# Optimization experiments

Measured on AMD Instinct MI355X. Metric: run time of the kernel, lower is better.

## Reference

```python
import jax, jax.numpy as jnp
import numpy as np

B, NP, NG = 4, 8192, 8192

def setup_inputs() -> dict:
    key = jax.random.key(0)
    k1, k2, k3 = jax.random.split(key, 3)
    pr_pts = jax.random.normal(k1, (B, NP, 3), dtype=jnp.float32)
    gt_pts = jax.random.normal(k2, (B, NG, 3), dtype=jnp.float32)
    gt_valid = jax.random.randint(k3, (B, NG), 0, 2) > 0
    return {"pr_pts": pr_pts, "gt_pts": gt_pts, "gt_valid": gt_valid}

def _sq_dists(a, b):
    # a: [B,N,3], b: [B,M,3] -> squared pairwise distances [B,N,M]
    a2 = jnp.sum(a * a, -1)  # [B,N]
    b2 = jnp.sum(b * b, -1)  # [B,M]
    ab = jnp.einsum('bnd,bmd->bnm', a, b)
    return a2[:, :, None] + b2[:, None, :] - 2.0 * ab

def reference(pr_pts, gt_pts, gt_valid):
    # Bidirectional Chamfer distance with gt validity mask.
    d2 = _sq_dists(pr_pts, gt_pts)  # [B,Np,Ng]
    # accuracy: for each predicted point, min squared dist to a VALID gt point
    d2_masked = jnp.where(gt_valid[:, None, :], d2, jnp.inf)
    acc_b = jnp.mean(jnp.min(d2_masked, axis=-1), axis=-1)  # [B]
    # completeness: for each valid gt point, min squared dist to any pred point
    min_over_pr = jnp.min(d2, axis=1)  # [B,Ng]
    valid_f = gt_valid.astype(min_over_pr.dtype)
    com_b = jnp.sum(min_over_pr * valid_f, axis=-1) / jnp.maximum(jnp.sum(valid_f, axis=-1), 1.0)
    loss_acc = jnp.mean(acc_b)
    loss_com = jnp.mean(com_b)
    loss_cd = loss_acc + loss_com
    # Sum((loss_acc,None),(loss_com,None),(loss_cd,None)) with scalar losses -> acc+com+cd
    return loss_acc + loss_com + loss_cd
```

## Files before the change

kernel.cpp:

```cpp
#include <hip/hip_runtime.h>

#define BB 4
#define NN 8192

typedef _Float16 f16;
typedef _Float16 f16x8 __attribute__((ext_vector_type(8)));
typedef float f32x16 __attribute__((ext_vector_type(16)));

#define SZ_PACK (BB * NN * 16)
#define OFF_PART_BYTES (4 * SZ_PACK * 2)
#define OFF_RES_BYTES (OFF_PART_BYTES + 16 * NN * 4)

__global__ __launch_bounds__(256) void k_init(
    const float* __restrict__ pr, const float* __restrict__ gt,
    const int* __restrict__ valid,
    f16* __restrict__ APR, f16* __restrict__ BGT,
    f16* __restrict__ AGT, f16* __restrict__ BPR,
    float* __restrict__ res) {
  int i = blockIdx.x * 256 + threadIdx.x;
  if (blockIdx.x == 0 && threadIdx.x < 16) res[threadIdx.x] = 0.0f;
  if (i >= BB * NN) return;
  float px = pr[3 * i], py = pr[3 * i + 1], pz = pr[3 * i + 2];
  float gx = gt[3 * i], gy = gt[3 * i + 1], gz = gt[3 * i + 2];
  int vld = valid[i] != 0;

  f16 phx = (f16)px, phy = (f16)py, phz = (f16)pz;
  f16 plx = (f16)(px - (float)phx), ply = (f16)(py - (float)phy), plz = (f16)(pz - (float)phz);
  float p2 = px * px + py * py + pz * pz;
  f16 p2h = (f16)p2, p2l = (f16)(p2 - (float)p2h);

  f16 ghx = (f16)gx, ghy = (f16)gy, ghz = (f16)gz;
  f16 glx = (f16)(gx - (float)ghx), gly = (f16)(gy - (float)ghy), glz = (f16)(gz - (float)ghz);
  float g2 = gx * gx + gy * gy + gz * gz;
  f16 g2h = (f16)g2, g2l = (f16)(g2 - (float)g2h);
  f16 g2hm = vld ? g2h : (f16)32768.0f;
  f16 g2lm = vld ? g2l : (f16)0.0f;

  const f16 one = (f16)1.0f, zero = (f16)0.0f;
  union Rec { f16 h[16]; uint4 u[2]; };

  Rec ra;
  ra.h[0] = (f16)(-2.f * (float)phx); ra.h[1] = (f16)(-2.f * (float)phy); ra.h[2] = (f16)(-2.f * (float)phz);
  ra.h[3] = ra.h[0]; ra.h[4] = ra.h[1]; ra.h[5] = ra.h[2];
  ra.h[6] = (f16)(-2.f * (float)plx); ra.h[7] = (f16)(-2.f * (float)ply); ra.h[8] = (f16)(-2.f * (float)plz);
  ra.h[9] = p2h; ra.h[10] = p2l; ra.h[11] = one; ra.h[12] = one;
  ra.h[13] = zero; ra.h[14] = zero; ra.h[15] = zero;
  ((uint4*)APR)[2 * i] = ra.u[0]; ((uint4*)APR)[2 * i + 1] = ra.u[1];

  Rec rb;
  rb.h[0] = phx; rb.h[1] = phy; rb.h[2] = phz;
  rb.h[3] = plx; rb.h[4] = ply; rb.h[5] = plz;
  rb.h[6] = phx; rb.h[7] = phy; rb.h[8] = phz;
  rb.h[9] = one; rb.h[10] = one; rb.h[11] = p2h; rb.h[12] = p2l;
  rb.h[13] = zero; rb.h[14] = zero; rb.h[15] = zero;
  ((uint4*)BPR)[2 * i] = rb.u[0]; ((uint4*)BPR)[2 * i + 1] = rb.u[1];

  Rec rc;
  rc.h[0] = (f16)(-2.f * (float)ghx); rc.h[1] = (f16)(-2.f * (float)ghy); rc.h[2] = (f16)(-2.f * (float)ghz);
  rc.h[3] = rc.h[0]; rc.h[4] = rc.h[1]; rc.h[5] = rc.h[2];
  rc.h[6] = (f16)(-2.f * (float)glx); rc.h[7] = (f16)(-2.f * (float)gly); rc.h[8] = (f16)(-2.f * (float)glz);
  rc.h[9] = g2h; rc.h[10] = g2l; rc.h[11] = one; rc.h[12] = one;
  rc.h[13] = zero; rc.h[14] = zero; rc.h[15] = zero;
  ((uint4*)AGT)[2 * i] = rc.u[0]; ((uint4*)AGT)[2 * i + 1] = rc.u[1];

  Rec rd;
  rd.h[0] = ghx; rd.h[1] = ghy; rd.h[2] = ghz;
  rd.h[3] = glx; rd.h[4] = gly; rd.h[5] = glz;
  rd.h[6] = ghx; rd.h[7] = ghy; rd.h[8] = ghz;
  rd.h[9] = one; rd.h[10] = one; rd.h[11] = g2hm; rd.h[12] = g2lm;
  rd.h[13] = zero; rd.h[14] = zero; rd.h[15] = zero;
  ((uint4*)BGT)[2 * i] = rd.u[0]; ((uint4*)BGT)[2 * i + 1] = rd.u[1];
}

__global__ __launch_bounds__(256, 4) void k_dist(
    const f16* __restrict__ APR, const f16* __restrict__ BGT,
    const f16* __restrict__ AGT, const f16* __restrict__ BPR,
    float* __restrict__ partial) {
  __shared__ f16 lds[2 * 1024 * 8];
  int id = blockIdx.x;
  int wgrow = id & 63;
  int half  = (id >> 6) & 1;
  int b     = (id >> 7) & 3;
  int p     = id >> 9;
  const f16* A  = p ? AGT : APR;
  const f16* Bv = p ? BPR : BGT;
  int tid = threadIdx.x;
  int wave = tid >> 6, lane = tid & 63;
  int nn = lane & 31, q = lane >> 5;

  const f16* Ab = A + ((size_t)b * NN + wgrow * 128 + wave * 32 + nn) * 16 + q * 8;
  f16x8 af = *(const f16x8*)Ab;

  f32x16 zc = {};
  f32x16 m;
#pragma unroll
  for (int i = 0; i < 16; ++i) m[i] = 1e38f;

  const uint4* gsrc = (const uint4*)(Bv + ((size_t)b * NN + half * 4096) * 16);
  uint4* ldsu = (uint4*)lds;
  const f16x8* lf = (const f16x8*)lds;

  for (int chunk = 0; chunk < 4; ++chunk) {
    const uint4* src = gsrc + (size_t)chunk * 2048;
#pragma unroll
    for (int k = 0; k < 8; ++k) {
      int u = tid + 256 * k;
      ldsu[(u & 1) * 1024 + (u >> 1)] = src[u];
    }
    __syncthreads();
    for (int t = 0; t < 32; t += 2) {
      f16x8 b0 = lf[q * 1024 + t * 32 + nn];
      f16x8 b1 = lf[q * 1024 + (t + 1) * 32 + nn];
      f32x16 d0 = __builtin_amdgcn_mfma_f32_32x32x16_f16(af, b0, zc, 0, 0, 0);
      f32x16 d1 = __builtin_amdgcn_mfma_f32_32x32x16_f16(af, b1, zc, 0, 0, 0);
#pragma unroll
      for (int i = 0; i < 16; ++i)
        m[i] = fminf(fminf(d0[i], d1[i]), m[i]);
    }
    __syncthreads();
  }

#pragma unroll
  for (int i = 0; i < 16; ++i) {
    float v = m[i];
    v = fminf(v, __shfl_xor(v, 1, 64));
    v = fminf(v, __shfl_xor(v, 2, 64));
    v = fminf(v, __shfl_xor(v, 4, 64));
    v = fminf(v, __shfl_xor(v, 8, 64));
    v = fminf(v, __shfl_xor(v, 16, 64));
    m[i] = fmaxf(v, 0.0f);
  }

  float* pb = partial + (((size_t)(p * 4 + b) * 2 + half) * NN) + wgrow * 128 + wave * 32;
#pragma unroll
  for (int reg = 0; reg < 16; ++reg) {
    int rit = (reg & 3) + 8 * (reg >> 2) + 4 * q;
    if ((lane & 31) == reg) pb[rit] = m[reg];
  }
}

__global__ __launch_bounds__(256) void k_red(
    const float* __restrict__ partial, const int* __restrict__ valid,
    float* __restrict__ res) {
  int g = blockIdx.x >> 3, seg = blockIdx.x & 7;
  int pp = g >> 2, bb = g & 3;
  int tid = threadIdx.x;
  const float* pb = partial + (size_t)g * 2 * NN;

  float sum = 0.0f, cnt = 0.0f;
#pragma unroll
  for (int k = 0; k < 4; ++k) {
    int r = seg * 1024 + tid + 256 * k;
    float v = fminf(pb[r], pb[NN + r]);
    if (pp == 0) {
      sum += v;
    } else {
      int vld = valid[bb * NN + r] != 0;
      sum += vld ? v : 0.0f;
      cnt += vld ? 1.0f : 0.0f;
    }
  }
  __shared__ float r1[256], r2[256];
  r1[tid] = sum; r2[tid] = cnt;
  __syncthreads();
  for (int off = 128; off > 0; off >>= 1) {
    if (tid < off) { r1[tid] += r1[tid + off]; r2[tid] += r2[tid + off]; }
    __syncthreads();
  }
  if (tid == 0) {
    if (pp == 0) {
      atomicAdd(&res[bb], r1[0]);
    } else {
      atomicAdd(&res[4 + bb], r1[0]);
      atomicAdd(&res[8 + bb], r2[0]);
    }
  }
}

__global__ void k_final(const float* __restrict__ res, float* __restrict__ out) {
  if (threadIdx.x == 0 && blockIdx.x == 0) {
    float a = 0.f, c = 0.f;
    for (int bb = 0; bb < 4; ++bb) {
      a += res[bb] / (float)NN;
      c += res[4 + bb] / fmaxf(res[8 + bb], 1.0f);
    }
    out[0] = 0.5f * (a + c);
  }
}

extern "C" void kernel_launch(void* const* d_in, const int* in_sizes, int n_in,
                              void* d_out, int out_size, void* d_ws, size_t ws_size,
                              hipStream_t stream) {
  const float* pr    = (const float*)d_in[0];
  const float* gt    = (const float*)d_in[1];
  const int*   valid = (const int*)d_in[2];

  f16* base = (f16*)d_ws;
  f16* APR = base;
  f16* BGT = base + SZ_PACK;
  f16* AGT = base + 2 * SZ_PACK;
  f16* BPR = base + 3 * SZ_PACK;
  float* partial = (float*)((char*)d_ws + OFF_PART_BYTES);
  float* res     = (float*)((char*)d_ws + OFF_RES_BYTES);

  k_init<<<(BB * NN) / 256, 256, 0, stream>>>(pr, gt, valid, APR, BGT, AGT, BPR, res);
  k_dist<<<1024, 256, 0, stream>>>(APR, BGT, AGT, BPR, partial);
  k_red<<<64, 256, 0, stream>>>(partial, valid, res);
  k_final<<<1, 64, 0, stream>>>(res, (float*)d_out);
}
```

Measured before the change: 89.84 us.

## Double rows per wave in k_dist and fold final reduction into k_red

Each wave now processes two 32-row A tiles against every B fragment read from LDS, which halves the LDS traffic and global B staging per output row. The grid shrinks from 1024 to 512 workgroups with launch bounds relaxed to 2 waves per SIMD, trading occupancy for register-level reuse. The separate k_final launch is removed: the last k_red block, detected with an atomic counter, computes the output. This saves one kernel launch but relies on res[12] being zeroed by k_init and adds threadfence and atomic reads.

New measurement: 91.94 us. +2.3%, slower.

```diff
diff --git a/kernel.cpp b/kernel.cpp
--- a/kernel.cpp
+++ b/kernel.cpp
@@ -72,29 +72,30 @@
   ((uint4*)BGT)[2 * i] = rd.u[0]; ((uint4*)BGT)[2 * i + 1] = rd.u[1];
 }
 
-__global__ __launch_bounds__(256, 4) void k_dist(
+__global__ __launch_bounds__(256, 2) void k_dist(
     const f16* __restrict__ APR, const f16* __restrict__ BGT,
     const f16* __restrict__ AGT, const f16* __restrict__ BPR,
     float* __restrict__ partial) {
   __shared__ f16 lds[2 * 1024 * 8];
   int id = blockIdx.x;
-  int wgrow = id & 63;
-  int half  = (id >> 6) & 1;
-  int b     = (id >> 7) & 3;
-  int p     = id >> 9;
+  int rowwg = id & 31;
+  int half  = (id >> 5) & 1;
+  int b     = (id >> 6) & 3;
+  int p     = id >> 8;
   const f16* A  = p ? AGT : APR;
   const f16* Bv = p ? BPR : BGT;
   int tid = threadIdx.x;
   int wave = tid >> 6, lane = tid & 63;
   int nn = lane & 31, q = lane >> 5;
 
-  const f16* Ab = A + ((size_t)b * NN + wgrow * 128 + wave * 32 + nn) * 16 + q * 8;
-  f16x8 af = *(const f16x8*)Ab;
+  const f16* Ab = A + ((size_t)b * NN + rowwg * 256 + wave * 64 + nn) * 16 + q * 8;
+  f16x8 af0 = *(const f16x8*)Ab;
+  f16x8 af1 = *(const f16x8*)(Ab + 32 * 16);
 
   f32x16 zc = {};
-  f32x16 m;
-#pragma unroll
-  for (int i = 0; i < 16; ++i) m[i] = 1e38f;
+  f32x16 m0, m1;
+#pragma unroll
+  for (int i = 0; i < 16; ++i) { m0[i] = 1e38f; m1[i] = 1e38f; }
 
   const uint4* gsrc = (const uint4*)(Bv + ((size_t)b * NN + half * 4096) * 16);
   uint4* ldsu = (uint4*)lds;
@@ -111,37 +112,49 @@
     for (int t = 0; t < 32; t += 2) {
       f16x8 b0 = lf[q * 1024 + t * 32 + nn];
       f16x8 b1 = lf[q * 1024 + (t + 1) * 32 + nn];
-      f32x16 d0 = __builtin_amdgcn_mfma_f32_32x32x16_f16(af, b0, zc, 0, 0, 0);
-      f32x16 d1 = __builtin_amdgcn_mfma_f32_32x32x16_f16(af, b1, zc, 0, 0, 0);
-#pragma unroll
-      for (int i = 0; i < 16; ++i)
-        m[i] = fminf(fminf(d0[i], d1[i]), m[i]);
+      f32x16 d00 = __builtin_amdgcn_mfma_f32_32x32x16_f16(af0, b0, zc, 0, 0, 0);
+      f32x16 d01 = __builtin_amdgcn_mfma_f32_32x32x16_f16(af0, b1, zc, 0, 0, 0);
+#pragma unroll
+      for (int i = 0; i < 16; ++i) m0[i] = fminf(fminf(d00[i], d01[i]), m0[i]);
+      f32x16 d10 = __builtin_amdgcn_mfma_f32_32x32x16_f16(af1, b0, zc, 0, 0, 0);
+      f32x16 d11 = __builtin_amdgcn_mfma_f32_32x32x16_f16(af1, b1, zc, 0, 0, 0);
+#pragma unroll
+      for (int i = 0; i < 16; ++i) m1[i] = fminf(fminf(d10[i], d11[i]), m1[i]);
     }
     __syncthreads();
   }
 
 #pragma unroll
   for (int i = 0; i < 16; ++i) {
-    float v = m[i];
-    v = fminf(v, __shfl_xor(v, 1, 64));
-    v = fminf(v, __shfl_xor(v, 2, 64));
-    v = fminf(v, __shfl_xor(v, 4, 64));
-    v = fminf(v, __shfl_xor(v, 8, 64));
-    v = fminf(v, __shfl_xor(v, 16, 64));
-    m[i] = fmaxf(v, 0.0f);
-  }
-
-  float* pb = partial + (((size_t)(p * 4 + b) * 2 + half) * NN) + wgrow * 128 + wave * 32;
+    float v0 = m0[i], v1 = m1[i];
+    v0 = fminf(v0, __shfl_xor(v0, 1, 64));
+    v1 = fminf(v1, __shfl_xor(v1, 1, 64));
+    v0 = fminf(v0, __shfl_xor(v0, 2, 64));
+    v1 = fminf(v1, __shfl_xor(v1, 2, 64));
+    v0 = fminf(v0, __shfl_xor(v0, 4, 64));
+    v1 = fminf(v1, __shfl_xor(v1, 4, 64));
+    v0 = fminf(v0, __shfl_xor(v0, 8, 64));
+    v1 = fminf(v1, __shfl_xor(v1, 8, 64));
+    v0 = fminf(v0, __shfl_xor(v0, 16, 64));
+    v1 = fminf(v1, __shfl_xor(v1, 16, 64));
+    m0[i] = fmaxf(v0, 0.0f);
+    m1[i] = fmaxf(v1, 0.0f);
+  }
+
+  float* pb = partial + (((size_t)(p * 4 + b) * 2 + half) * NN) + rowwg * 256 + wave * 64;
 #pragma unroll
   for (int reg = 0; reg < 16; ++reg) {
     int rit = (reg & 3) + 8 * (reg >> 2) + 4 * q;
-    if ((lane & 31) == reg) pb[rit] = m[reg];
+    if ((lane & 31) == reg) {
+      pb[rit] = m0[reg];
+      pb[32 + rit] = m1[reg];
+    }
   }
 }
 
 __global__ __launch_bounds__(256) void k_red(
     const float* __restrict__ partial, const int* __restrict__ valid,
-    float* __restrict__ res) {
+    float* __restrict__ res, float* __restrict__ out) {
   int g = blockIdx.x >> 3, seg = blockIdx.x & 7;
   int pp = g >> 2, bb = g & 3;
   int tid = threadIdx.x;
@@ -174,17 +187,19 @@
       atomicAdd(&res[4 + bb], r1[0]);
       atomicAdd(&res[8 + bb], r2[0]);
     }
-  }
-}
-
-__global__ void k_final(const float* __restrict__ res, float* __restrict__ out) {
-  if (threadIdx.x == 0 && blockIdx.x == 0) {
-    float a = 0.f, c = 0.f;
-    for (int bb = 0; bb < 4; ++bb) {
-      a += res[bb] / (float)NN;
-      c += res[4 + bb] / fmaxf(res[8 + bb], 1.0f);
-    }
-    out[0] = 0.5f * (a + c);
+    __threadfence();
+    int done = atomicAdd((int*)&res[12], 1);
+    if (done == 63) {
+      float a = 0.f, c = 0.f;
+      for (int B2 = 0; B2 < 4; ++B2) {
+        float tA = atomicAdd(&res[B2], 0.0f);
+        float tC = atomicAdd(&res[4 + B2], 0.0f);
+        float tN = atomicAdd(&res[8 + B2], 0.0f);
+        a += tA / (float)NN;
+        c += tC / fmaxf(tN, 1.0f);
+      }
+      out[0] = 0.5f * (a + c);
+    }
   }
 }
 
@@ -204,7 +219,6 @@
   float* res     = (float*)((char*)d_ws + OFF_RES_BYTES);
 
   k_init<<<(BB * NN) / 256, 256, 0, stream>>>(pr, gt, valid, APR, BGT, AGT, BPR, res);
-  k_dist<<<1024, 256, 0, stream>>>(APR, BGT, AGT, BPR, partial);
-  k_red<<<64, 256, 0, stream>>>(partial, valid, res);
-  k_final<<<1, 64, 0, stream>>>(res, (float*)d_out);
-}
+  k_dist<<<512, 256, 0, stream>>>(APR, BGT, AGT, BPR, partial);
+  k_red<<<64, 256, 0, stream>>>(partial, valid, res, (float*)d_out);
+}
```
